# Kernel tuning notes

Hardware: AMD Instinct MI355X
Metric: run time of the kernel (lower is better)

The kernel has to match this reference:

```python
import math
import jax, jax.numpy as jnp
import numpy as np

THETA = 2 ** 16

def _get_freqs(n: int) -> jnp.ndarray:
    # positions quantized to multiples of 2 (pairs share a frequency)
    pos = jnp.floor(jnp.arange(n, dtype=jnp.float32) / 2.0) * 2.0
    return 1.0 / (THETA ** (pos / n)) / (2.0 * math.pi)  # (n,)

def _rope(phases: jnp.ndarray, v: jnp.ndarray) -> jnp.ndarray:
    # phases in 'cycles'; wrap to [0,1) then scale to radians
    ph = (phases % 1.0) * (2.0 * math.pi)
    c, s = jnp.cos(ph), jnp.sin(ph)
    # interleaved rotate-half: out[..., 2i] = -v[..., 2i+1], out[..., 2i+1] = v[..., 2i]
    v_rot = jnp.stack((-v[..., 1::2], v[..., ::2]), axis=-1).reshape(v.shape)
    return (v * c).astype(v.dtype) + (v_rot * s).astype(v.dtype)


def setup_inputs() -> dict:
    key = jax.random.key(0)
    kq, kv = jax.random.split(key)
    B, H, T, N, D = 2, 8, 2048, 1024, 128
    Q = jax.random.normal(kq, (B, H, T, N), dtype=jnp.float32)
    K = Q  # module asserts K is Q
    V = jax.random.normal(kv, (B, H, T, D), dtype=jnp.float32)
    return {"Q": Q, "K": K, "V": V}


def reference(Q, K, V):
    B, H, T, N = Q.shape
    freqs = _get_freqs(N)  # (N,)
    # r_phases: (T, N) = position * freq (broadcast over B, H)
    r_phases = jnp.arange(T, dtype=jnp.float32)[:, None] * freqs[None, :]
    QR = _rope(r_phases, Q)  # (B,H,T,N); KR = QR since K is Q
    scores = jnp.einsum('bhtn,bhsn->bhts', QR, QR)  # (B,H,T,T)
    causal = jnp.tril(jnp.ones((T, T), dtype=bool), k=-1)  # strict lower triangle
    scores = jnp.where(causal, scores, 0.0)
    return jnp.einsum('bhts,bhsd->bhtd', scores, V)  # (B,H,T,D)
```

## Files before the change

kernel.cpp:

```cpp
#include <hip/hip_runtime.h>

typedef __bf16 bf16_t;
typedef bf16_t bf16x8 __attribute__((ext_vector_type(8)));
typedef float f32x4 __attribute__((ext_vector_type(4)));
typedef unsigned short u16;
typedef unsigned int u32;

#define T_DIM 2048
#define N_DIM 1024
#define D_DIM 128

__device__ __forceinline__ u16 f32_to_bf16(float f) {
    u32 u = __builtin_bit_cast(u32, f);
    u += 0x7FFFu + ((u >> 16) & 1u);
    return (u16)(u >> 16);
}
__device__ __forceinline__ float bf16_to_f32(u16 v) {
    u32 u = (u32)v << 16;
    return __builtin_bit_cast(float, u);
}

typedef __attribute__((address_space(1))) const u32 guint;
typedef __attribute__((address_space(3))) u32 luint;
__device__ __forceinline__ void stage16(const void* g, void* l) {
    __builtin_amdgcn_global_load_lds((guint*)g, (luint*)l, 16, 0, 0);
}
__device__ __forceinline__ void wait_vm0_barrier() {
    asm volatile("s_waitcnt vmcnt(0)" ::: "memory");
    __builtin_amdgcn_s_barrier();
}

__global__ void ropet_kernel(const float* __restrict__ Q, u16* __restrict__ QR,
                             u16* __restrict__ QRt) {
    __shared__ u16 til[64][65];
    const int bh  = blockIdx.x >> 9;
    const int rem = blockIdx.x & 511;
    const int t0 = (rem >> 4) * 64, n0 = (rem & 15) * 64;
    const float* src = Q + (size_t)bh * ((size_t)T_DIM * N_DIM) + (size_t)t0 * N_DIM + n0;
    u16* qdst = QR + (size_t)bh * ((size_t)T_DIM * N_DIM) + (size_t)t0 * N_DIM + n0;
    #pragma unroll
    for (int k = 0; k < 4; ++k) {
        const int linear = k * 256 + threadIdx.x;
        const int r = linear >> 4;
        const int f = linear & 15;
        const float4 q = *(const float4*)(src + (size_t)r * N_DIM + f * 4);
        const int t = t0 + r;
        u16 o[4];
        #pragma unroll
        for (int pp = 0; pp < 2; ++pp) {
            const int pidx = ((n0 + f * 4) >> 1) + pp;
            const float freq = exp2f((float)pidx * (-1.0f / 32.0f)) * 0.15915494309189535f;
            float ph = (float)t * freq;
            ph -= floorf(ph);
            const float s = __builtin_amdgcn_sinf(ph);
            const float c = __builtin_amdgcn_cosf(ph);
            const float a  = pp ? q.z : q.x;
            const float b2 = pp ? q.w : q.y;
            o[2 * pp]     = f32_to_bf16(a * c - b2 * s);
            o[2 * pp + 1] = f32_to_bf16(b2 * c + a * s);
        }
        *(uint2*)(qdst + (size_t)r * N_DIM + f * 4) = *(const uint2*)o;
        til[r][f * 4 + 0] = o[0]; til[r][f * 4 + 1] = o[1];
        til[r][f * 4 + 2] = o[2]; til[r][f * 4 + 3] = o[3];
    }
    __syncthreads();
    u16* tdst = QRt + (size_t)bh * ((size_t)N_DIM * T_DIM) + (size_t)n0 * T_DIM + t0;
    #pragma unroll
    for (int k = 0; k < 2; ++k) {
        const int linear = k * 256 + threadIdx.x;
        const int nl = linear >> 3, o = linear & 7;
        u16 tmp[8];
        #pragma unroll
        for (int e = 0; e < 8; ++e) tmp[e] = til[o * 8 + e][nl];
        *(uint4*)(tdst + (size_t)nl * T_DIM + o * 8) = *(const uint4*)tmp;
    }
}

__global__ void vt_kernel(const float* __restrict__ V, u16* __restrict__ Vt) {
    __shared__ u16 tile[64][65];
    const int bh   = blockIdx.x >> 6;
    const int rem  = blockIdx.x & 63;
    const int t0 = (rem >> 1) * 64, d0 = (rem & 1) * 64;
    const float* src = V + ((size_t)bh * T_DIM + t0) * D_DIM + d0;
    #pragma unroll
    for (int k = 0; k < 16; ++k) {
        int linear = k * 256 + threadIdx.x;
        int r = linear >> 6, c = linear & 63;
        tile[r][c] = f32_to_bf16(src[(size_t)r * D_DIM + c]);
    }
    __syncthreads();
    u16* dst = Vt + ((size_t)bh * D_DIM + d0) * T_DIM + t0;
    #pragma unroll
    for (int k = 0; k < 16; ++k) {
        int linear = k * 256 + threadIdx.x;
        int dr = linear >> 6, tc = linear & 63;
        dst[(size_t)dr * T_DIM + tc] = tile[tc][dr];
    }
}

__global__ __launch_bounds__(256, 1)
void statescan_kernel(const u16* __restrict__ QRt, const u16* __restrict__ Vt,
                      u16* __restrict__ UP) {
    __shared__ __align__(16) u16 Smem[24576];

    const int b  = blockIdx.x;
    const int bh = b >> 4;
    const int nt = (b >> 1) & 7;
    const int dt = b & 1;

    const int tid  = threadIdx.x;
    const int w    = tid >> 6;
    const int wy   = w >> 1, wx = w & 1;
    const int lane = tid & 63;
    const int quad = lane >> 4;
    const int l15  = lane & 15;
    const int sw   = l15 & 7;
    const int srow = lane >> 3;
    const int scol = (lane & 7) ^ (srow & 7);

    const u16* Ag = Vt  + (size_t)bh * ((size_t)D_DIM * T_DIM) + (size_t)(dt * 64)  * T_DIM;
    const u16* Bg = QRt + (size_t)bh * ((size_t)N_DIM * T_DIM) + (size_t)(nt * 128) * T_DIM;

    const f32x4 fz = {0.f, 0.f, 0.f, 0.f};
    f32x4 acc[2][4];
    #pragma unroll
    for (int mi = 0; mi < 2; ++mi)
        #pragma unroll
        for (int nj = 0; nj < 4; ++nj)
            acc[mi][nj] = fz;

    auto STAGE = [&](int buf, int s) {
        const int toff = s * 64;
        #pragma unroll
        for (int ia = 0; ia < 2; ++ia)
            stage16(Ag + (size_t)(w * 16 + ia * 8 + srow) * T_DIM + toff + scol * 8,
                    Smem + buf * 4096 + (w * 16 + ia * 8) * 64);
        #pragma unroll
        for (int ib = 0; ib < 4; ++ib)
            stage16(Bg + (size_t)(w * 32 + ib * 8 + srow) * T_DIM + toff + scol * 8,
                    Smem + 8192 + buf * 8192 + (w * 32 + ib * 8) * 64);
    };

    u16* upb = UP + (size_t)(bh * 16) * (128 * (size_t)N_DIM)
                  + (size_t)(dt * 64) * N_DIM + nt * 128;

    auto WRITE_UP = [&](int ci) {
        u16* ub = upb + (size_t)ci * (128 * (size_t)N_DIM);
        #pragma unroll
        for (int mi = 0; mi < 2; ++mi)
            #pragma unroll
            for (int nj = 0; nj < 4; ++nj)
                #pragma unroll
                for (int rr = 0; rr < 4; ++rr)
                    ub[(size_t)(wy * 32 + mi * 16 + quad * 4 + rr) * N_DIM + wx * 64 + nj * 16 + l15]
                        = f32_to_bf16(acc[mi][nj][rr]);
    };

    STAGE(0, 0);
    wait_vm0_barrier();
    int buf = 0;
    for (int s = 0; s < 30; ++s) {
        if ((s & 1) == 0) WRITE_UP(s >> 1);
        if (s < 29) STAGE(buf ^ 1, s + 1);
        const char* As = (const char*)(Smem + buf * 4096);
        const char* Bs = (const char*)(Smem + 8192 + buf * 8192);
        #pragma unroll
        for (int kc = 0; kc < 2; ++kc) {
            bf16x8 af[2], bfr[4];
            #pragma unroll
            for (int mi = 0; mi < 2; ++mi)
                af[mi] = *(const bf16x8*)(As + (wy * 32 + mi * 16 + l15) * 128 + (((kc * 4 + quad) ^ sw) << 4));
            #pragma unroll
            for (int nj = 0; nj < 4; ++nj)
                bfr[nj] = *(const bf16x8*)(Bs + (wx * 64 + nj * 16 + l15) * 128 + (((kc * 4 + quad) ^ sw) << 4));
            #pragma unroll
            for (int mi = 0; mi < 2; ++mi)
                #pragma unroll
                for (int nj = 0; nj < 4; ++nj)
                    acc[mi][nj] = __builtin_amdgcn_mfma_f32_16x16x32_bf16(af[mi], bfr[nj], acc[mi][nj], 0, 0, 0);
        }
        wait_vm0_barrier();
        buf ^= 1;
    }
    WRITE_UP(15);
}

__global__ __launch_bounds__(256, 1)
void attn3_kernel(const u16* __restrict__ QR, const u16* __restrict__ UP,
                  const u16* __restrict__ Vt, float* __restrict__ Out) {
    __shared__ __align__(16) u16 Smem[32768];
    u16 (*Ps)[140] = (u16 (*)[140])Smem;

    const int b  = blockIdx.x;
    const int bh = b >> 4;
    const int i  = b & 15;

    const int tid  = threadIdx.x;
    const int w    = tid >> 6;
    const int wy   = w >> 1, wx = w & 1;
    const int lane = tid & 63;
    const int quad = lane >> 4;
    const int l15  = lane & 15;
    const int sw   = l15 & 7;
    const int srow = lane >> 3;
    const int scol = (lane & 7) ^ (srow & 7);

    const u16* Ap = QR + (size_t)bh * ((size_t)T_DIM * N_DIM)
                       + (size_t)(i * 128 + w * 32 + srow) * N_DIM + scol * 8;
    const u16* Bp = UP + (size_t)(b * 128 + w * 32 + srow) * N_DIM + scol * 8;

    const f32x4 fz = {0.f, 0.f, 0.f, 0.f};
    f32x4 sm[4][4], si[4][4];
    #pragma unroll
    for (int mi = 0; mi < 4; ++mi)
        #pragma unroll
        for (int nj = 0; nj < 4; ++nj) {
            sm[mi][nj] = fz;
            si[mi][nj] = fz;
        }

    auto STAGE = [&](int buf, int kk16) {
        const int kk = kk16 * 64;
        #pragma unroll
        for (int ii = 0; ii < 4; ++ii) {
            stage16(Ap + (size_t)(ii * 8) * N_DIM + kk, Smem + buf * 8192 + (w * 32 + ii * 8) * 64);
            stage16(Bp + (size_t)(ii * 8) * N_DIM + kk, Smem + 16384 + buf * 8192 + (w * 32 + ii * 8) * 64);
        }
    };

    STAGE(0, 0);
    wait_vm0_barrier();
    int buf = 0;
    for (int kk16 = 0; kk16 < 16; ++kk16) {
        if (kk16 < 15) STAGE(buf ^ 1, kk16 + 1);
        const char* As = (const char*)(Smem + buf * 8192);
        const char* Bs = (const char*)(Smem + 16384 + buf * 8192);
        #pragma unroll
        for (int kc = 0; kc < 2; ++kc) {
            bf16x8 af[4], bm[4], bi[4];
            #pragma unroll
            for (int mi = 0; mi < 4; ++mi)
                af[mi] = *(const bf16x8*)(As + (wy * 64 + mi * 16 + l15) * 128 + (((kc * 4 + quad) ^ sw) << 4));
            #pragma unroll
            for (int nj = 0; nj < 4; ++nj) {
                bm[nj] = *(const bf16x8*)(Bs + (wx * 64 + nj * 16 + l15) * 128 + (((kc * 4 + quad) ^ sw) << 4));
                bi[nj] = *(const bf16x8*)(As + (wx * 64 + nj * 16 + l15) * 128 + (((kc * 4 + quad) ^ sw) << 4));
            }
            #pragma unroll
            for (int mi = 0; mi < 4; ++mi)
                #pragma unroll
                for (int nj = 0; nj < 4; ++nj) {
                    sm[mi][nj] = __builtin_amdgcn_mfma_f32_16x16x32_bf16(af[mi], bm[nj], sm[mi][nj], 0, 0, 0);
                    si[mi][nj] = __builtin_amdgcn_mfma_f32_16x16x32_bf16(af[mi], bi[nj], si[mi][nj], 0, 0, 0);
                }
        }
        wait_vm0_barrier();
        buf ^= 1;
    }

    #pragma unroll
    for (int mi = 0; mi < 4; ++mi) {
        const int rowb = wy * 64 + mi * 16 + quad * 4;
        #pragma unroll
        for (int nj = 0; nj < 4; ++nj) {
            const int col = wx * 64 + nj * 16 + l15;
            #pragma unroll
            for (int rr = 0; rr < 4; ++rr)
                if (col >= rowb + rr) si[mi][nj][rr] = 0.f;
        }
    }
    #pragma unroll
    for (int mi = 0; mi < 4; ++mi) {
        const int rowb = wy * 64 + mi * 16 + quad * 4;
        #pragma unroll
        for (int nj = 0; nj < 4; ++nj) {
            const int col = wx * 64 + nj * 16 + l15;
            #pragma unroll
            for (int rr = 0; rr < 4; ++rr)
                Ps[rowb + rr][col] = f32_to_bf16(si[mi][nj][rr]);
        }
    }
    __syncthreads();

    const u16* vjb = Vt + (size_t)bh * ((size_t)D_DIM * T_DIM)
                        + (size_t)(wx * 64 + l15) * T_DIM + i * 128 + quad * 8;
    #pragma unroll
    for (int kc = 0; kc < 4; ++kc) {
        bf16x8 pf[4];
        #pragma unroll
        for (int mi = 0; mi < 4; ++mi)
            pf[mi] = *(const bf16x8*)(&Ps[wy * 64 + mi * 16 + l15][kc * 32 + quad * 8]);
        #pragma unroll
        for (int nj = 0; nj < 4; ++nj) {
            const bf16x8 vv = *(const bf16x8*)(vjb + (size_t)(nj * 16) * T_DIM + kc * 32);
            #pragma unroll
            for (int mi = 0; mi < 4; ++mi)
                sm[mi][nj] = __builtin_amdgcn_mfma_f32_16x16x32_bf16(pf[mi], vv, sm[mi][nj], 0, 0, 0);
        }
    }

    float* ob = Out + ((size_t)bh * T_DIM + (size_t)i * 128) * D_DIM;
    #pragma unroll
    for (int mi = 0; mi < 4; ++mi)
        #pragma unroll
        for (int nj = 0; nj < 4; ++nj)
            #pragma unroll
            for (int rr = 0; rr < 4; ++rr)
                ob[(size_t)(wy * 64 + mi * 16 + quad * 4 + rr) * D_DIM + wx * 64 + nj * 16 + l15]
                    = sm[mi][nj][rr];
}

__global__ void rope_kernel(const float* __restrict__ Q, u16* __restrict__ QR) {
    const int g = blockIdx.x * 256 + threadIdx.x;
    const int base = g * 4;
    const int t  = (base >> 9) & (T_DIM - 1);
    const int p0 = base & 511;
    const float4 qa = ((const float4*)Q)[g * 2];
    const float4 qb = ((const float4*)Q)[g * 2 + 1];
    const float vin[4][2] = {{qa.x, qa.y}, {qa.z, qa.w}, {qb.x, qb.y}, {qb.z, qb.w}};
    u16 ov[8];
    #pragma unroll
    for (int uu = 0; uu < 4; ++uu) {
        const float freq = exp2f((float)(p0 + uu) * (-1.0f / 32.0f)) * 0.15915494309189535f;
        float ph = (float)t * freq;
        ph = ph - floorf(ph);
        const float s = __builtin_amdgcn_sinf(ph);
        const float c = __builtin_amdgcn_cosf(ph);
        ov[2 * uu]     = f32_to_bf16(vin[uu][0] * c - vin[uu][1] * s);
        ov[2 * uu + 1] = f32_to_bf16(vin[uu][1] * c + vin[uu][0] * s);
    }
    ((uint4*)QR)[g] = *(const uint4*)ov;
}

__device__ __forceinline__ int run_start(int b) { return b < 128 ? 5 * b : 640 + 4 * (b - 128); }

__global__ __launch_bounds__(256, 2)
void attn_kernel(const u16* __restrict__ QR, const u16* __restrict__ Vt,
                 float* __restrict__ Out, u16* __restrict__ Part) {
    __shared__ __align__(16) u16 Smem[17920];
    u16 (*As)[64]  = (u16 (*)[64])Smem;
    u16 (*Bs)[64]  = (u16 (*)[64])(Smem + 8192);
    u16 (*Ps)[140] = (u16 (*)[140])Smem;

    const int b     = blockIdx.x;
    const int start = run_start(b);
    const int len   = b < 128 ? 5 : 4;

    const int tid  = threadIdx.x;
    const int w    = tid >> 6;
    const int wy   = w >> 1, wx = w & 1;
    const int lane = tid & 63;
    const int quad = lane >> 4;
    const int l15  = lane & 15;
    const int sw   = l15 & 7;
    const int srow = lane >> 3;
    const int scol = (lane & 7) ^ (srow & 7);

    const f32x4 fz = {0.f, 0.f, 0.f, 0.f};
    f32x4 o_acc[4][4];
    int cur_bh = -1, cur_qt = -1;
    bool hasj0 = false;
    const u16* QRb = QR;
    const u16* Ap  = QR;
    const u16* Vb  = Vt;

    for (int it = 0; it < len; ++it) {
        const int i = start + it;
        const int bh = i / 136;
        const int r  = i - bh * 136;
        int qt = 15, j = 0, acc = 0;
        #pragma unroll 1
        for (int q = 0; q < 16; ++q) {
            if (r < acc + q + 1) { qt = q; j = r - acc; break; }
            acc += q + 1;
        }

        if (qt != cur_qt || bh != cur_bh) {
            if (cur_qt >= 0) {
                if (hasj0) {
                    float* ob = Out + ((size_t)cur_bh * T_DIM + (size_t)cur_qt * 128) * D_DIM;
                    #pragma unroll
                    for (int mi = 0; mi < 4; ++mi)
                        #pragma unroll
                        for (int nj = 0; nj < 4; ++nj)
                            #pragma unroll
                            for (int rr = 0; rr < 4; ++rr)
                                ob[(size_t)(wy * 64 + mi * 16 + quad * 4 + rr) * D_DIM + wx * 64 + nj * 16 + l15] = o_acc[mi][nj][rr];
                } else {
                    u16* pb = Part + (size_t)b * 16384;
                    #pragma unroll
                    for (int mi = 0; mi < 4; ++mi)
                        #pragma unroll
                        for (int nj = 0; nj < 4; ++nj)
                            #pragma unroll
                            for (int rr = 0; rr < 4; ++rr)
                                pb[(wy * 64 + mi * 16 + quad * 4 + rr) * 128 + wx * 64 + nj * 16 + l15] = f32_to_bf16(o_acc[mi][nj][rr]);
                }
            }
            cur_bh = bh; cur_qt = qt; hasj0 = (j == 0);
            #pragma unroll
            for (int mi = 0; mi < 4; ++mi)
                #pragma unroll
                for (int nj = 0; nj < 4; ++nj)
                    o_acc[mi][nj] = fz;
            QRb = QR + (size_t)bh * (T_DIM * N_DIM);
            Ap  = QRb + (size_t)(qt * 128 + w * 32 + srow) * N_DIM + scol * 8;
            Vb  = Vt + (size_t)bh * (D_DIM * T_DIM) + (size_t)(wx * 64 + l15) * T_DIM + quad * 8;
        }

        const u16* Bp = QRb + (size_t)(j * 128 + w * 32 + srow) * N_DIM + scol * 8;
        f32x4 s_acc[4][4];
        #pragma unroll
        for (int mi = 0; mi < 4; ++mi)
            #pragma unroll
            for (int nj = 0; nj < 4; ++nj)
                s_acc[mi][nj] = fz;

        __syncthreads();

        for (int kk = 0; kk < N_DIM; kk += 64) {
            #pragma unroll
            for (int ii = 0; ii < 4; ++ii) {
                stage16(Ap + (size_t)ii * 8 * N_DIM + kk, &As[w * 32 + ii * 8][0]);
                stage16(Bp + (size_t)ii * 8 * N_DIM + kk, &Bs[w * 32 + ii * 8][0]);
            }
            __syncthreads();
            #pragma unroll
            for (int kc = 0; kc < 2; ++kc) {
                bf16x8 af[4], bfr[4];
                #pragma unroll
                for (int mi = 0; mi < 4; ++mi)
                    af[mi] = *(const bf16x8*)((const char*)As + (wy * 64 + mi * 16 + l15) * 128 + (((kc * 4 + quad) ^ sw) << 4));
                #pragma unroll
                for (int nj = 0; nj < 4; ++nj)
                    bfr[nj] = *(const bf16x8*)((const char*)Bs + (wx * 64 + nj * 16 + l15) * 128 + (((kc * 4 + quad) ^ sw) << 4));
                #pragma unroll
                for (int mi = 0; mi < 4; ++mi)
                    #pragma unroll
                    for (int nj = 0; nj < 4; ++nj)
                        s_acc[mi][nj] = __builtin_amdgcn_mfma_f32_16x16x32_bf16(af[mi], bfr[nj], s_acc[mi][nj], 0, 0, 0);
            }
            __syncthreads();
        }

        if (j == qt) {
            #pragma unroll
            for (int mi = 0; mi < 4; ++mi) {
                const int rowb = wy * 64 + mi * 16 + quad * 4;
                #pragma unroll
                for (int nj = 0; nj < 4; ++nj) {
                    const int col = wx * 64 + nj * 16 + l15;
                    #pragma unroll
                    for (int rr = 0; rr < 4; ++rr)
                        if (col >= rowb + rr) s_acc[mi][nj][rr] = 0.f;
                }
            }
        }

        #pragma unroll
        for (int mi = 0; mi < 4; ++mi) {
            const int rowb = wy * 64 + mi * 16 + quad * 4;
            #pragma unroll
            for (int nj = 0; nj < 4; ++nj) {
                const int col = wx * 64 + nj * 16 + l15;
                #pragma unroll
                for (int rr = 0; rr < 4; ++rr)
                    Ps[rowb + rr][col] = f32_to_bf16(s_acc[mi][nj][rr]);
            }
        }
        __syncthreads();

        const u16* vjb = Vb + j * 128;
        #pragma unroll
        for (int kc = 0; kc < 4; ++kc) {
            bf16x8 pf[4];
            #pragma unroll
            for (int mi = 0; mi < 4; ++mi)
                pf[mi] = *(const bf16x8*)(&Ps[wy * 64 + mi * 16 + l15][kc * 32 + quad * 8]);
            #pragma unroll
            for (int nj = 0; nj < 4; ++nj) {
                const bf16x8 vv = *(const bf16x8*)(vjb + (size_t)(nj * 16) * T_DIM + kc * 32);
                #pragma unroll
                for (int mi = 0; mi < 4; ++mi)
                    o_acc[mi][nj] = __builtin_amdgcn_mfma_f32_16x16x32_bf16(pf[mi], vv, o_acc[mi][nj], 0, 0, 0);
            }
        }
    }

    if (hasj0) {
        float* ob = Out + ((size_t)cur_bh * T_DIM + (size_t)cur_qt * 128) * D_DIM;
        #pragma unroll
        for (int mi = 0; mi < 4; ++mi)
            #pragma unroll
            for (int nj = 0; nj < 4; ++nj)
                #pragma unroll
                for (int rr = 0; rr < 4; ++rr)
                    ob[(size_t)(wy * 64 + mi * 16 + quad * 4 + rr) * D_DIM + wx * 64 + nj * 16 + l15] = o_acc[mi][nj][rr];
    } else {
        u16* pb = Part + (size_t)b * 16384;
        #pragma unroll
        for (int mi = 0; mi < 4; ++mi)
            #pragma unroll
            for (int nj = 0; nj < 4; ++nj)
                #pragma unroll
                for (int rr = 0; rr < 4; ++rr)
                    pb[(wy * 64 + mi * 16 + quad * 4 + rr) * 128 + wx * 64 + nj * 16 + l15] = f32_to_bf16(o_acc[mi][nj][rr]);
    }
}

__global__ void combine_kernel(float* __restrict__ Out, const u16* __restrict__ Part) {
    const int bh = blockIdx.x & 15;
    const int qt = 1 + (blockIdx.x >> 4);
    const int ts = bh * 136 + (qt * (qt + 1)) / 2;
    const int lo = ts + 1, hi = ts + qt;
    int bmin = (lo <= 640) ? (lo + 4) / 5 : 128 + (lo - 640 + 3) / 4;
    int writers[4], nw = 0;
    for (int bb = bmin; bb < 512 && run_start(bb) <= hi && nw < 4; ++bb)
        writers[nw++] = bb;
    if (nw == 0) return;
    float* ob = Out + ((size_t)bh * T_DIM + (size_t)qt * 128) * D_DIM;
    const int tid = threadIdx.x;
    #pragma unroll 1
    for (int e = 0; e < 64; ++e) {
        const int idx = e * 256 + tid;
        float a = ob[idx];
        for (int k = 0; k < nw; ++k)
            a += bf16_to_f32(Part[(size_t)writers[k] * 16384 + idx]);
        ob[idx] = a;
    }
}

extern "C" void kernel_launch(void* const* d_in, const int* in_sizes, int n_in,
                              void* d_out, int out_size, void* d_ws, size_t ws_size,
                              hipStream_t stream) {
    const float* Q = (const float*)d_in[0];
    const float* V = (const float*)d_in[2];
    float* Out = (float*)d_out;

    const size_t QR_E = (size_t)16 * T_DIM * N_DIM;
    const size_t VT_E = (size_t)16 * D_DIM * T_DIM;
    const size_t UP_E = (size_t)256 * 128 * N_DIM;
    const size_t need = (QR_E * 2 + VT_E + UP_E) * 2;

    if (ws_size >= need) {
        u16* QRw  = (u16*)d_ws;
        u16* QRtw = QRw + QR_E;
        u16* Vtw  = QRtw + QR_E;
        u16* UPw  = Vtw + VT_E;

        ropet_kernel<<<dim3(8192), dim3(256), 0, stream>>>(Q, QRw, QRtw);
        vt_kernel<<<dim3(1024), dim3(256), 0, stream>>>(V, Vtw);
        statescan_kernel<<<dim3(256), dim3(256), 0, stream>>>(QRtw, Vtw, UPw);
        attn3_kernel<<<dim3(256), dim3(256), 0, stream>>>(QRw, UPw, Vtw, Out);
    } else {
        u16* QRw  = (u16*)d_ws;
        u16* Vtw  = QRw + QR_E;
        u16* Part = Vtw + VT_E;

        rope_kernel<<<dim3(16384), dim3(256), 0, stream>>>(Q, QRw);
        vt_kernel<<<dim3(1024), dim3(256), 0, stream>>>(V, Vtw);
        attn_kernel<<<dim3(512), dim3(256), 0, stream>>>(QRw, Vtw, Out, Part);
        combine_kernel<<<dim3(240), dim3(256), 0, stream>>>(Out, Part);
    }
}
```

Baseline: 365.1 us.

## Split GEMM kernels across eight waves and widen RoPE-transpose tiles

The statescan and attn3 kernels now launch 512 threads per block instead of 256. Each wave owns half as many output rows, which cuts accumulator registers per wave and doubles the waves available to hide latency. attn3 also remaps block indices so that co-scheduled blocks interleave across heads, and ropet now handles 64x128 tiles with 16-byte vector LDS writes and an XOR swizzle in place of the padded 65-wide tile. In exchange, each wave does less MFMA work per LDS fragment load, and barriers now synchronise more waves.

```diff
diff --git a/kernel.cpp b/kernel.cpp
--- a/kernel.cpp
+++ b/kernel.cpp
@@ -32,47 +32,48 @@
 
 __global__ void ropet_kernel(const float* __restrict__ Q, u16* __restrict__ QR,
                              u16* __restrict__ QRt) {
-    __shared__ u16 til[64][65];
-    const int bh  = blockIdx.x >> 9;
-    const int rem = blockIdx.x & 511;
-    const int t0 = (rem >> 4) * 64, n0 = (rem & 15) * 64;
+    __shared__ __align__(16) u16 til[64][136];
+    const int bh  = blockIdx.x >> 8;
+    const int rem = blockIdx.x & 255;
+    const int t0 = (rem >> 3) * 64, n0 = (rem & 7) * 128;
     const float* src = Q + (size_t)bh * ((size_t)T_DIM * N_DIM) + (size_t)t0 * N_DIM + n0;
     u16* qdst = QR + (size_t)bh * ((size_t)T_DIM * N_DIM) + (size_t)t0 * N_DIM + n0;
     #pragma unroll
     for (int k = 0; k < 4; ++k) {
-        const int linear = k * 256 + threadIdx.x;
-        const int r = linear >> 4;
-        const int f = linear & 15;
-        const float4 q = *(const float4*)(src + (size_t)r * N_DIM + f * 4);
+        const int slot = k * 256 + threadIdx.x;
+        const int r  = slot >> 4;
+        const int f8 = slot & 15;
+        const float4 qa = *(const float4*)(src + (size_t)r * N_DIM + f8 * 8);
+        const float4 qb = *(const float4*)(src + (size_t)r * N_DIM + f8 * 8 + 4);
+        const float vin[4][2] = {{qa.x, qa.y}, {qa.z, qa.w}, {qb.x, qb.y}, {qb.z, qb.w}};
         const int t = t0 + r;
-        u16 o[4];
-        #pragma unroll
-        for (int pp = 0; pp < 2; ++pp) {
-            const int pidx = ((n0 + f * 4) >> 1) + pp;
+        u16 ov[8];
+        #pragma unroll
+        for (int pp = 0; pp < 4; ++pp) {
+            const int pidx = (n0 >> 1) + f8 * 4 + pp;
             const float freq = exp2f((float)pidx * (-1.0f / 32.0f)) * 0.15915494309189535f;
             float ph = (float)t * freq;
             ph -= floorf(ph);
             const float s = __builtin_amdgcn_sinf(ph);
             const float c = __builtin_amdgcn_cosf(ph);
-            const float a  = pp ? q.z : q.x;
-            const float b2 = pp ? q.w : q.y;
-            o[2 * pp]     = f32_to_bf16(a * c - b2 * s);
-            o[2 * pp + 1] = f32_to_bf16(b2 * c + a * s);
-        }
-        *(uint2*)(qdst + (size_t)r * N_DIM + f * 4) = *(const uint2*)o;
-        til[r][f * 4 + 0] = o[0]; til[r][f * 4 + 1] = o[1];
-        til[r][f * 4 + 2] = o[2]; til[r][f * 4 + 3] = o[3];
+            ov[2 * pp]     = f32_to_bf16(vin[pp][0] * c - vin[pp][1] * s);
+            ov[2 * pp + 1] = f32_to_bf16(vin[pp][1] * c + vin[pp][0] * s);
+        }
+        *(uint4*)(qdst + (size_t)r * N_DIM + f8 * 8) = *(const uint4*)ov;
+        *(uint4*)(&til[r][(f8 * 8) ^ (((r >> 3) & 7) << 3)]) = *(const uint4*)ov;
     }
     __syncthreads();
     u16* tdst = QRt + (size_t)bh * ((size_t)N_DIM * T_DIM) + (size_t)n0 * T_DIM + t0;
     #pragma unroll
-    for (int k = 0; k < 2; ++k) {
-        const int linear = k * 256 + threadIdx.x;
-        const int nl = linear >> 3, o = linear & 7;
-        u16 tmp[8];
-        #pragma unroll
-        for (int e = 0; e < 8; ++e) tmp[e] = til[o * 8 + e][nl];
-        *(uint4*)(tdst + (size_t)nl * T_DIM + o * 8) = *(const uint4*)tmp;
+    for (int k = 0; k < 4; ++k) {
+        const int slot = k * 256 + threadIdx.x;
+        const int nl = slot >> 3;
+        const int t8 = slot & 7;
+        u16 ov2[8];
+        #pragma unroll
+        for (int e = 0; e < 8; ++e)
+            ov2[e] = til[t8 * 8 + e][nl ^ (t8 << 3)];
+        *(uint4*)(tdst + (size_t)nl * T_DIM + t8 * 8) = *(const uint4*)ov2;
     }
 }
 
@@ -98,7 +99,7 @@
     }
 }
 
-__global__ __launch_bounds__(256, 1)
+__global__ __launch_bounds__(512, 2)
 void statescan_kernel(const u16* __restrict__ QRt, const u16* __restrict__ Vt,
                       u16* __restrict__ UP) {
     __shared__ __align__(16) u16 Smem[24576];
@@ -122,23 +123,22 @@
     const u16* Bg = QRt + (size_t)bh * ((size_t)N_DIM * T_DIM) + (size_t)(nt * 128) * T_DIM;
 
     const f32x4 fz = {0.f, 0.f, 0.f, 0.f};
-    f32x4 acc[2][4];
-    #pragma unroll
-    for (int mi = 0; mi < 2; ++mi)
-        #pragma unroll
-        for (int nj = 0; nj < 4; ++nj)
-            acc[mi][nj] = fz;
+    f32x4 acc[4];
+    #pragma unroll
+    for (int nj = 0; nj < 4; ++nj) acc[nj] = fz;
 
     auto STAGE = [&](int buf, int s) {
         const int toff = s * 64;
-        #pragma unroll
-        for (int ia = 0; ia < 2; ++ia)
-            stage16(Ag + (size_t)(w * 16 + ia * 8 + srow) * T_DIM + toff + scol * 8,
-                    Smem + buf * 4096 + (w * 16 + ia * 8) * 64);
-        #pragma unroll
-        for (int ib = 0; ib < 4; ++ib)
-            stage16(Bg + (size_t)(w * 32 + ib * 8 + srow) * T_DIM + toff + scol * 8,
-                    Smem + 8192 + buf * 8192 + (w * 32 + ib * 8) * 64);
+        if (w < 4) {
+            #pragma unroll
+            for (int ia = 0; ia < 2; ++ia)
+                stage16(Ag + (size_t)(w * 16 + ia * 8 + srow) * T_DIM + toff + scol * 8,
+                        Smem + buf * 4096 + (w * 16 + ia * 8) * 64);
+        }
+        #pragma unroll
+        for (int ib = 0; ib < 2; ++ib)
+            stage16(Bg + (size_t)(w * 16 + ib * 8 + srow) * T_DIM + toff + scol * 8,
+                    Smem + 8192 + buf * 8192 + (w * 16 + ib * 8) * 64);
     };
 
     u16* upb = UP + (size_t)(bh * 16) * (128 * (size_t)N_DIM)
@@ -147,13 +147,11 @@
     auto WRITE_UP = [&](int ci) {
         u16* ub = upb + (size_t)ci * (128 * (size_t)N_DIM);
         #pragma unroll
-        for (int mi = 0; mi < 2; ++mi)
-            #pragma unroll
-            for (int nj = 0; nj < 4; ++nj)
-                #pragma unroll
-                for (int rr = 0; rr < 4; ++rr)
-                    ub[(size_t)(wy * 32 + mi * 16 + quad * 4 + rr) * N_DIM + wx * 64 + nj * 16 + l15]
-                        = f32_to_bf16(acc[mi][nj][rr]);
+        for (int nj = 0; nj < 4; ++nj)
+            #pragma unroll
+            for (int rr = 0; rr < 4; ++rr)
+                ub[(size_t)(wy * 16 + quad * 4 + rr) * N_DIM + wx * 64 + nj * 16 + l15]
+                    = f32_to_bf16(acc[nj][rr]);
     };
 
     STAGE(0, 0);
@@ -166,18 +164,14 @@
         const char* Bs = (const char*)(Smem + 8192 + buf * 8192);
         #pragma unroll
         for (int kc = 0; kc < 2; ++kc) {
-            bf16x8 af[2], bfr[4];
-            #pragma unroll
-            for (int mi = 0; mi < 2; ++mi)
-                af[mi] = *(const bf16x8*)(As + (wy * 32 + mi * 16 + l15) * 128 + (((kc * 4 + quad) ^ sw) << 4));
+            bf16x8 af, bfr[4];
+            af = *(const bf16x8*)(As + (wy * 16 + l15) * 128 + (((kc * 4 + quad) ^ sw) << 4));
             #pragma unroll
             for (int nj = 0; nj < 4; ++nj)
                 bfr[nj] = *(const bf16x8*)(Bs + (wx * 64 + nj * 16 + l15) * 128 + (((kc * 4 + quad) ^ sw) << 4));
             #pragma unroll
-            for (int mi = 0; mi < 2; ++mi)
-                #pragma unroll
-                for (int nj = 0; nj < 4; ++nj)
-                    acc[mi][nj] = __builtin_amdgcn_mfma_f32_16x16x32_bf16(af[mi], bfr[nj], acc[mi][nj], 0, 0, 0);
+            for (int nj = 0; nj < 4; ++nj)
+                acc[nj] = __builtin_amdgcn_mfma_f32_16x16x32_bf16(af, bfr[nj], acc[nj], 0, 0, 0);
         }
         wait_vm0_barrier();
         buf ^= 1;
@@ -185,13 +179,13 @@
     WRITE_UP(15);
 }
 
-__global__ __launch_bounds__(256, 1)
+__global__ __launch_bounds__(512, 2)
 void attn3_kernel(const u16* __restrict__ QR, const u16* __restrict__ UP,
                   const u16* __restrict__ Vt, float* __restrict__ Out) {
     __shared__ __align__(16) u16 Smem[32768];
     u16 (*Ps)[140] = (u16 (*)[140])Smem;
 
-    const int b  = blockIdx.x;
+    const int b  = (blockIdx.x & 7) * 32 + (blockIdx.x >> 3);
     const int bh = b >> 4;
     const int i  = b & 15;
 
@@ -206,13 +200,13 @@
     const int scol = (lane & 7) ^ (srow & 7);
 
     const u16* Ap = QR + (size_t)bh * ((size_t)T_DIM * N_DIM)
-                       + (size_t)(i * 128 + w * 32 + srow) * N_DIM + scol * 8;
-    const u16* Bp = UP + (size_t)(b * 128 + w * 32 + srow) * N_DIM + scol * 8;
+                       + (size_t)(i * 128 + w * 16 + srow) * N_DIM + scol * 8;
+    const u16* Bp = UP + (size_t)(b * 128 + w * 16 + srow) * N_DIM + scol * 8;
 
     const f32x4 fz = {0.f, 0.f, 0.f, 0.f};
-    f32x4 sm[4][4], si[4][4];
-    #pragma unroll
-    for (int mi = 0; mi < 4; ++mi)
+    f32x4 sm[2][4], si[2][4];
+    #pragma unroll
+    for (int mi = 0; mi < 2; ++mi)
         #pragma unroll
         for (int nj = 0; nj < 4; ++nj) {
             sm[mi][nj] = fz;
@@ -222,9 +216,9 @@
     auto STAGE = [&](int buf, int kk16) {
         const int kk = kk16 * 64;
         #pragma unroll
-        for (int ii = 0; ii < 4; ++ii) {
-            stage16(Ap + (size_t)(ii * 8) * N_DIM + kk, Smem + buf * 8192 + (w * 32 + ii * 8) * 64);
-            stage16(Bp + (size_t)(ii * 8) * N_DIM + kk, Smem + 16384 + buf * 8192 + (w * 32 + ii * 8) * 64);
+        for (int ii = 0; ii < 2; ++ii) {
+            stage16(Ap + (size_t)(ii * 8) * N_DIM + kk, Smem + buf * 8192 + (w * 16 + ii * 8) * 64);
+            stage16(Bp + (size_t)(ii * 8) * N_DIM + kk, Smem + 16384 + buf * 8192 + (w * 16 + ii * 8) * 64);
         }
     };
 
@@ -237,17 +231,17 @@
         const char* Bs = (const char*)(Smem + 16384 + buf * 8192);
         #pragma unroll
         for (int kc = 0; kc < 2; ++kc) {
-            bf16x8 af[4], bm[4], bi[4];
-            #pragma unroll
-            for (int mi = 0; mi < 4; ++mi)
-                af[mi] = *(const bf16x8*)(As + (wy * 64 + mi * 16 + l15) * 128 + (((kc * 4 + quad) ^ sw) << 4));
+            bf16x8 af[2], bm[4], bi[4];
+            #pragma unroll
+            for (int mi = 0; mi < 2; ++mi)
+                af[mi] = *(const bf16x8*)(As + (wy * 32 + mi * 16 + l15) * 128 + (((kc * 4 + quad) ^ sw) << 4));
             #pragma unroll
             for (int nj = 0; nj < 4; ++nj) {
                 bm[nj] = *(const bf16x8*)(Bs + (wx * 64 + nj * 16 + l15) * 128 + (((kc * 4 + quad) ^ sw) << 4));
                 bi[nj] = *(const bf16x8*)(As + (wx * 64 + nj * 16 + l15) * 128 + (((kc * 4 + quad) ^ sw) << 4));
             }
             #pragma unroll
-            for (int mi = 0; mi < 4; ++mi)
+            for (int mi = 0; mi < 2; ++mi)
                 #pragma unroll
                 for (int nj = 0; nj < 4; ++nj) {
                     sm[mi][nj] = __builtin_amdgcn_mfma_f32_16x16x32_bf16(af[mi], bm[nj], sm[mi][nj], 0, 0, 0);
@@ -259,8 +253,8 @@
     }
 
     #pragma unroll
-    for (int mi = 0; mi < 4; ++mi) {
-        const int rowb = wy * 64 + mi * 16 + quad * 4;
+    for (int mi = 0; mi < 2; ++mi) {
+        const int rowb = wy * 32 + mi * 16 + quad * 4;
         #pragma unroll
         for (int nj = 0; nj < 4; ++nj) {
             const int col = wx * 64 + nj * 16 + l15;
@@ -270,8 +264,8 @@
         }
     }
     #pragma unroll
-    for (int mi = 0; mi < 4; ++mi) {
-        const int rowb = wy * 64 + mi * 16 + quad * 4;
+    for (int mi = 0; mi < 2; ++mi) {
+        const int rowb = wy * 32 + mi * 16 + quad * 4;
         #pragma unroll
         for (int nj = 0; nj < 4; ++nj) {
             const int col = wx * 64 + nj * 16 + l15;
@@ -286,27 +280,27 @@
                         + (size_t)(wx * 64 + l15) * T_DIM + i * 128 + quad * 8;
     #pragma unroll
     for (int kc = 0; kc < 4; ++kc) {
-        bf16x8 pf[4];
-        #pragma unroll
-        for (int mi = 0; mi < 4; ++mi)
-            pf[mi] = *(const bf16x8*)(&Ps[wy * 64 + mi * 16 + l15][kc * 32 + quad * 8]);
+        bf16x8 pf[2];
+        #pragma unroll
+        for (int mi = 0; mi < 2; ++mi)
+            pf[mi] = *(const bf16x8*)(&Ps[wy * 32 + mi * 16 + l15][kc * 32 + quad * 8]);
         #pragma unroll
         for (int nj = 0; nj < 4; ++nj) {
             const bf16x8 vv = *(const bf16x8*)(vjb + (size_t)(nj * 16) * T_DIM + kc * 32);
             #pragma unroll
-            for (int mi = 0; mi < 4; ++mi)
+            for (int mi = 0; mi < 2; ++mi)
                 sm[mi][nj] = __builtin_amdgcn_mfma_f32_16x16x32_bf16(pf[mi], vv, sm[mi][nj], 0, 0, 0);
         }
     }
 
     float* ob = Out + ((size_t)bh * T_DIM + (size_t)i * 128) * D_DIM;
     #pragma unroll
-    for (int mi = 0; mi < 4; ++mi)
+    for (int mi = 0; mi < 2; ++mi)
         #pragma unroll
         for (int nj = 0; nj < 4; ++nj)
             #pragma unroll
             for (int rr = 0; rr < 4; ++rr)
-                ob[(size_t)(wy * 64 + mi * 16 + quad * 4 + rr) * D_DIM + wx * 64 + nj * 16 + l15]
+                ob[(size_t)(wy * 32 + mi * 16 + quad * 4 + rr) * D_DIM + wx * 64 + nj * 16 + l15]
                     = sm[mi][nj][rr];
 }
 
@@ -548,10 +542,10 @@
         u16* Vtw  = QRtw + QR_E;
         u16* UPw  = Vtw + VT_E;
 
-        ropet_kernel<<<dim3(8192), dim3(256), 0, stream>>>(Q, QRw, QRtw);
+        ropet_kernel<<<dim3(4096), dim3(256), 0, stream>>>(Q, QRw, QRtw);
         vt_kernel<<<dim3(1024), dim3(256), 0, stream>>>(V, Vtw);
-        statescan_kernel<<<dim3(256), dim3(256), 0, stream>>>(QRtw, Vtw, UPw);
-        attn3_kernel<<<dim3(256), dim3(256), 0, stream>>>(QRw, UPw, Vtw, Out);
+        statescan_kernel<<<dim3(256), dim3(512), 0, stream>>>(QRtw, Vtw, UPw);
+        attn3_kernel<<<dim3(256), dim3(512), 0, stream>>>(QRw, UPw, Vtw, Out);
     } else {
         u16* QRw  = (u16*)d_ws;
         u16* Vtw  = QRw + QR_E;
```

New measurement: 362.9 us. About the same (-0.6%).
